# Kernel optimization log

Measured on AMD Instinct MI355X. Metric: run time of the kernel, lower is better.

## Reference

```python
import jax, jax.numpy as jnp
import numpy as np

SCALE = 2  # init_kwargs scale


def _splits(a, s):
    # (..., W, H) -> (..., W//s, H//s, s*s), matching torch view/permute order
    *lead, W, H = a.shape
    Ws, Hs = W // s, H // s
    n = len(lead)
    b = a.reshape(*lead, s, Ws, s, Hs)
    b = jnp.transpose(b, tuple(range(n)) + (n + 1, n + 3, n, n + 2))
    return b.reshape(*lead, Ws, Hs, s * s)


def _p2o(psf, shape):
    # point-spread-function -> optical transfer function (zero-pad, center-roll, fft2)
    k1, k2 = psf.shape[-2], psf.shape[-1]
    otf = jnp.zeros(psf.shape[:-2] + shape, psf.dtype).at[..., :k1, :k2].set(psf)
    otf = jnp.roll(otf, (-(k1 // 2), -(k2 // 2)), axis=(-2, -1))
    return jnp.fft.fft2(otf, axes=(-2, -1))


def _upsample_zeros(x, s):
    if s == 1:
        return x
    B, C, H, W = x.shape
    return jnp.zeros((B, C, H * s, W * s), x.dtype).at[..., ::s, ::s].set(x)


def setup_inputs() -> dict:
    key = jax.random.key(0)
    k1, k2 = jax.random.split(key)
    B, C, H, W, K = 4, 64, 128, 128, 5
    x = jax.random.normal(k1, (B, C, H, W), jnp.float32)
    w = jax.random.normal(k2, (1, C, K, K), jnp.float32)
    # module init applies softmax over flattened kernel
    weight = jax.nn.softmax(w.reshape(1, C, -1), axis=-1).reshape(1, C, K, K)
    bias = jnp.zeros((1, C, 1, 1), jnp.float32)
    lambda_reg = jnp.full((1, 1, 1, 1), 0.1, jnp.float32)
    return {"x": x, "weight": weight, "bias": bias, "lambda_reg": lambda_reg}


def reference(x, weight, bias, lambda_reg):
    s = SCALE
    _, _, h, w = x.shape
    STy = _upsample_zeros(x, s)                      # [B,C,h*s,w*s] zero-interleaved
    if s != 1:
        x0 = jnp.repeat(jnp.repeat(x, s, axis=-2), s, axis=-1)  # nearest interp
    else:
        x0 = x
    FB = _p2o(weight, (h * s, w * s))                # [1,C,hs,ws] complex
    FBC = jnp.conj(FB)
    F2B = jnp.abs(FB) ** 2
    FBFy = FBC * jnp.fft.fft2(STy, axes=(-2, -1))
    FR = FBFy + jnp.fft.fft2(lambda_reg * x0, axes=(-2, -1))
    FBR = jnp.mean(_splits(FB * FR, s), axis=-1)     # [B,C,h,w] complex
    invW = jnp.mean(_splits(F2B, s), axis=-1)        # [1,C,h,w] real
    lambda_small = lambda_reg                        # scalar lambda: no split needed
    invWBR = FBR / (invW + lambda_small)
    FCBinvWBR = FBC * jnp.tile(invWBR, (1, 1, s, s))
    FX = (FR - FCBinvWBR) / lambda_reg
    out = jnp.real(jnp.fft.ifft2(FX, axes=(-2, -1)))
    return out + bias
```

## Files before the change

kernel.cpp:

```cpp
#include <hip/hip_runtime.h>
#include <math.h>


struct cx { float x, y; };
__device__ __forceinline__ cx cmul(cx a, cx b){ return cx{a.x*b.x - a.y*b.y, a.x*b.y + a.y*b.x}; }
__device__ __forceinline__ cx cadd(cx a, cx b){ return cx{a.x+b.x, a.y+b.y}; }
__device__ __forceinline__ cx csub(cx a, cx b){ return cx{a.x-b.x, a.y-b.y}; }
__device__ __forceinline__ cx cconj(cx a){ return cx{a.x, -a.y}; }
__device__ __forceinline__ cx cscale(cx a, float s){ return cx{a.x*s, a.y*s}; }

__device__ __forceinline__ float2 cmulf(float2 a, float2 b){
    return make_float2(a.x*b.x - a.y*b.y, a.x*b.y + a.y*b.x);
}
__device__ __forceinline__ float2 cmulcf(float2 a, float2 b){
    return make_float2(a.x*b.x + a.y*b.y, a.y*b.x - a.x*b.y);
}
__device__ __forceinline__ float2 caddf(float2 a, float2 b){ return make_float2(a.x+b.x, a.y+b.y); }
__device__ __forceinline__ float2 csubf(float2 a, float2 b){ return make_float2(a.x-b.x, a.y-b.y); }

__device__ __forceinline__ void barrier_lds(){
    __builtin_amdgcn_sched_barrier(0);
    asm volatile("s_waitcnt lgkmcnt(0)" ::: "memory");
    __builtin_amdgcn_s_barrier();
    __builtin_amdgcn_sched_barrier(0);
}

__global__ __launch_bounds__(256)
void precompute_K(const float* __restrict__ weight, const float* __restrict__ lam_ptr,
                  float2* __restrict__ KA, float2* __restrict__ KB)
{
    __shared__ float2 P[5 * 256];

    const int tid  = threadIdx.x;
    const int c    = blockIdx.x >> 5;
    const int slab = blockIdx.x & 31;

    const float* wc = weight + c*25;
    const float lam = lam_ptr[0];
    const float th  = -6.28318530717958647692f * (1.0f/256.0f);

    {
        float s1,c1, s2,c2;
        __sincosf(th * (float)tid,     &s1, &c1);
        __sincosf(th * (float)(2*tid), &s2, &c2);
        cx er[5] = { cx{c2,-s2}, cx{c1,-s1}, cx{1.f,0.f}, cx{c1,s1}, cx{c2,s2} };
        const int rs = (tid >> 1) | ((tid & 1) << 7);
        #pragma unroll
        for (int a = 0; a < 5; ++a) {
            float px = 0.f, py = 0.f;
            #pragma unroll
            for (int b = 0; b < 5; ++b) {
                float w = wc[a*5 + b];
                px += w * er[b].x;
                py += w * er[b].y;
            }
            P[a*256 + rs] = make_float2(px, py);
        }
    }
    __syncthreads();

    const float scale = 1.0f / 65536.0f;

    #pragma unroll 1
    for (int it = 0; it < 2; ++it) {
        const int p  = slab*512 + it*256 + tid;
        const int qb = p >> 7, rb = p & 127;
        const int q = (int)(__brev((unsigned)qb) >> 25);
        const int r = (int)(__brev((unsigned)rb) >> 25);
        const int rr = (r >> 1) | ((r & 1) << 7);

        float sq1,cq1, sq2,cq2;
        __sincosf(th * (float)q,     &sq1, &cq1);
        __sincosf(th * (float)(2*q), &sq2, &cq2);
        cx eq[5] = { cx{cq2,-sq2}, cx{cq1,-sq1}, cx{1.f,0.f}, cx{cq1,sq1}, cx{cq2,sq2} };

        cx F00{0.f,0.f}, F01{0.f,0.f}, F10{0.f,0.f}, F11{0.f,0.f};
        #pragma unroll
        for (int a = 0; a < 5; ++a) {
            float2 p0 = P[a*256 + rr];
            float2 p1 = P[a*256 + rr + 64];
            cx t0 = cmul(eq[a], cx{p0.x, p0.y});
            cx t1 = cmul(eq[a], cx{p1.x, p1.y});
            F00 = cadd(F00, t0); F01 = cadd(F01, t1);
            if (a & 1) { F10 = csub(F10, t0); F11 = csub(F11, t1); }
            else       { F10 = cadd(F10, t0); F11 = cadd(F11, t1); }
        }

        const float cq = cq1, sq = sq1, cr = 0.f, sr = 0.f;
        (void)cr; (void)sr;
        float sr1, cr1;
        __sincosf(th * (float)r, &sr1, &cr1);

        cx Du[2] = { cx{1.f+cq,  sq}, cx{1.f-cq, -sq} };
        cx Dv[2] = { cx{1.f+cr1,  sr1}, cx{1.f-cr1, -sr1} };
        cx Fm[2][2] = { {F00, F01}, {F10, F11} };
        cx R[2][2];
        float invW = 0.f;
        cx M{0.f,0.f};
        #pragma unroll
        for (int i = 0; i < 2; ++i)
          #pragma unroll
          for (int k = 0; k < 2; ++k) {
            cx fb = Fm[i][k];
            cx Rik = cadd(cconj(fb), cscale(cmul(Du[i], Dv[k]), lam));
            R[i][k] = Rik;
            invW += 0.25f * (fb.x*fb.x + fb.y*fb.y);
            M = cadd(M, cscale(cmul(fb, Rik), 0.25f));
          }
        cx V = cscale(M, 1.0f / (invW + lam));
        float inv_lam = 1.0f / lam;
        cx G[2][2];
        #pragma unroll
        for (int i = 0; i < 2; ++i)
          #pragma unroll
          for (int k = 0; k < 2; ++k)
            G[i][k] = cscale(csub(R[i][k], cmul(cconj(Fm[i][k]), V)), inv_lam);

        cx G00 = G[0][0], G01 = G[0][1], G10 = G[1][0], G11 = G[1][1];
        cx Gh00 = cadd(cadd(G00,G01), cadd(G10,G11));
        cx Gh01 = cadd(csub(G00,G01), csub(G10,G11));
        cx Gh10 = csub(cadd(G00,G01), cadd(G10,G11));
        cx Gh11 = csub(csub(G00,G01), csub(G10,G11));
        cx phq = cx{cq, -sq};
        cx phr = cx{cr1, -sr1};
        cx H0 = Gh00;
        cx H1 = cmul(Gh01, phr);
        cx H2 = cmul(Gh10, phq);
        cx H3 = cmul(Gh11, cmul(phq, phr));

        float2 kAv = make_float2((H0.x - H1.y)*scale, (H0.y + H1.x)*scale);
        float2 kBv = make_float2((H2.x - H3.y)*scale, (H2.y + H3.x)*scale);
        const int o = (c << 14) + p;
        KA[o] = kAv;
        KB[o] = kBv;
    }
}

#define ST2 129

template<int AXIS> __device__ __forceinline__ int laddr(int line, int i){
    return AXIS ? (i*ST2 + line) : (line*ST2 + i);
}

template<int AXIS, int S>
__device__ __forceinline__ void fwd_pair(float2* Sm, const float2* TW, int tid)
{
    const int h  = 64 >> S;
    const int hh = 32 >> S;
    #pragma unroll
    for (int it = 0; it < 4; ++it) {
        int qid  = it*1024 + tid;
        int line = qid & 127;
        int t    = qid >> 7;
        int blk  = t >> (5 - S);
        int j    = t & (hh - 1);
        int i0   = (blk << (7 - S)) + j;
        int a0 = laddr<AXIS>(line, i0);
        int a1 = laddr<AXIS>(line, i0 + hh);
        int a2 = laddr<AXIS>(line, i0 + h);
        int a3 = laddr<AXIS>(line, i0 + h + hh);
        float2 e0 = Sm[a0], e1 = Sm[a1], e2 = Sm[a2], e3 = Sm[a3];
        float2 w0 = TW[j << S], w1 = TW[(j << S) + 32], w2 = TW[j << (S + 1)];
        float2 u0 = caddf(e0, e2), d0 = cmulf(csubf(e0, e2), w0);
        float2 u1 = caddf(e1, e3), d1 = cmulf(csubf(e1, e3), w1);
        Sm[a0] = caddf(u0, u1);
        Sm[a1] = cmulf(csubf(u0, u1), w2);
        Sm[a2] = caddf(d0, d1);
        Sm[a3] = cmulf(csubf(d0, d1), w2);
    }
}

template<int AXIS, int S>
__device__ __forceinline__ void inv_pair(float2* Sm, const float2* TW, int tid)
{
    const int h = 1 << S;
    #pragma unroll
    for (int it = 0; it < 4; ++it) {
        int qid  = it*1024 + tid;
        int line = qid & 127;
        int t    = qid >> 7;
        int blk  = t >> S;
        int j    = t & (h - 1);
        int base = (blk << (S + 2)) + j;
        int a0 = laddr<AXIS>(line, base);
        int a1 = laddr<AXIS>(line, base + h);
        int a2 = laddr<AXIS>(line, base + 2*h);
        int a3 = laddr<AXIS>(line, base + 3*h);
        float2 e0 = Sm[a0], e1 = Sm[a1], e2 = Sm[a2], e3 = Sm[a3];
        float2 cw0 = TW[j << (6 - S)];
        float2 cw1 = TW[j << (5 - S)];
        float2 cw2 = TW[(j << (5 - S)) + 32];
        float2 t1 = cmulcf(e1, cw0);
        float2 A0 = caddf(e0, t1), A1 = csubf(e0, t1);
        float2 t2 = cmulcf(e3, cw0);
        float2 A2 = caddf(e2, t2), A3 = csubf(e2, t2);
        float2 u = cmulcf(A2, cw1);
        Sm[a0] = caddf(A0, u);
        Sm[a2] = csubf(A0, u);
        float2 v = cmulcf(A3, cw2);
        Sm[a1] = caddf(A1, v);
        Sm[a3] = csubf(A1, v);
    }
}

__global__ __launch_bounds__(1024)
void converse_main(const float* __restrict__ x, const float* __restrict__ bias,
                   const float2* __restrict__ KA, const float2* __restrict__ KB,
                   float* __restrict__ out)
{
    __shared__ float2 S[128 * ST2];
    __shared__ float2 TW[64];

    const int tid = threadIdx.x;
    const int bc  = blockIdx.x;
    const int c   = bc & 63;

    if (tid < 64) {
        float s_, c_;
        __sincosf(-6.28318530717958647692f * (float)tid * (1.0f/128.0f), &s_, &c_);
        TW[tid] = make_float2(c_, s_);
    }

    const float* xp = x + (size_t)bc * 16384;
    #pragma unroll
    for (int it = 0; it < 16; ++it) {
        int n = it * 1024 + tid;
        S[(n >> 7) * ST2 + (n & 127)] = make_float2(xp[n], 0.0f);
    }

    const float2* KpA = KA + (size_t)c * 16384;
    const float2* KpB = KB + (size_t)c * 16384;
    const int nn = tid & 127;
    const int t7 = tid >> 7;
    const int kbase = t7*256 + nn;
    float2 kr[16];
    #pragma unroll
    for (int it = 0; it < 8; ++it) {
        kr[2*it]   = KpA[it*2048 + kbase];
        kr[2*it+1] = KpA[it*2048 + kbase + 128];
    }
    barrier_lds();

    fwd_pair<0,0>(S, TW, tid); barrier_lds();
    fwd_pair<0,2>(S, TW, tid); barrier_lds();
    fwd_pair<0,4>(S, TW, tid); barrier_lds();
    #pragma unroll
    for (int it = 0; it < 8; ++it) {
        int g = it*1024 + tid;
        int line = g & 127, k = g >> 7;
        int a = line*ST2 + 2*k;
        float2 u = S[a], v = S[a+1];
        S[a]   = caddf(u, v);
        S[a+1] = csubf(u, v);
    }
    barrier_lds();

    fwd_pair<1,0>(S, TW, tid); barrier_lds();
    fwd_pair<1,2>(S, TW, tid); barrier_lds();
    fwd_pair<1,4>(S, TW, tid); barrier_lds();

    const float bv = bias[c];
    float* op = out + (size_t)bc * 65536;

    float2 sA[8], sB[8];
    #pragma unroll
    for (int it = 0; it < 8; ++it) {
        int j = it*8 + t7;
        int a = (2*j)*ST2 + nn;
        float2 u = S[a], v = S[a + ST2];
        float2 vA = caddf(u, v);
        float2 vB = csubf(u, v);
        sA[it] = vA;
        sB[it] = vB;
        float2 w0 = cmulf(vA, kr[2*it]);
        float2 w1 = cmulf(vB, kr[2*it+1]);
        S[a]       = caddf(w0, w1);
        S[a + ST2] = csubf(w0, w1);
    }
    barrier_lds();

    inv_pair<1,1>(S, TW, tid); barrier_lds();
    inv_pair<1,3>(S, TW, tid); barrier_lds();
    inv_pair<1,5>(S, TW, tid); barrier_lds();
    inv_pair<0,0>(S, TW, tid); barrier_lds();
    inv_pair<0,2>(S, TW, tid); barrier_lds();
    inv_pair<0,4>(S, TW, tid); barrier_lds();

    #pragma unroll
    for (int it = 0; it < 8; ++it) {
        int g = it*1024 + tid;
        int j = g & 63, m = g >> 6;
        int a = m*ST2 + j;
        float2 u = S[a], v = S[a + 64];
        float2 t = cmulcf(v, TW[j]);
        float2 o0 = caddf(u, t);
        float2 o1 = csubf(u, t);
        size_t ro = (size_t)(2*m) * 256;
        *(float2*)(op + ro + 2*j)       = make_float2(o0.x + bv, o0.y + bv);
        *(float2*)(op + ro + 2*j + 128) = make_float2(o1.x + bv, o1.y + bv);
    }
    barrier_lds();

    #pragma unroll
    for (int it = 0; it < 8; ++it) {
        int j = it*8 + t7;
        float2 kb0 = KpB[it*2048 + kbase];
        float2 kb1 = KpB[it*2048 + kbase + 128];
        float2 w0 = cmulf(sA[it], kb0);
        float2 w1 = cmulf(sB[it], kb1);
        int a = (2*j)*ST2 + nn;
        S[a]       = caddf(w0, w1);
        S[a + ST2] = csubf(w0, w1);
    }
    barrier_lds();

    inv_pair<1,1>(S, TW, tid); barrier_lds();
    inv_pair<1,3>(S, TW, tid); barrier_lds();
    inv_pair<1,5>(S, TW, tid); barrier_lds();
    inv_pair<0,0>(S, TW, tid); barrier_lds();
    inv_pair<0,2>(S, TW, tid); barrier_lds();
    inv_pair<0,4>(S, TW, tid); barrier_lds();

    #pragma unroll
    for (int it = 0; it < 8; ++it) {
        int g = it*1024 + tid;
        int j = g & 63, m = g >> 6;
        int a = m*ST2 + j;
        float2 u = S[a], v = S[a + 64];
        float2 t = cmulcf(v, TW[j]);
        float2 o0 = caddf(u, t);
        float2 o1 = csubf(u, t);
        size_t ro = (size_t)(2*m + 1) * 256;
        *(float2*)(op + ro + 2*j)       = make_float2(o0.x + bv, o0.y + bv);
        *(float2*)(op + ro + 2*j + 128) = make_float2(o1.x + bv, o1.y + bv);
    }
}

extern "C" void kernel_launch(void* const* d_in, const int* in_sizes, int n_in,
                              void* d_out, int out_size, void* d_ws, size_t ws_size,
                              hipStream_t stream)
{
    const float* x      = (const float*)d_in[0];
    const float* weight = (const float*)d_in[1];
    const float* bias   = (const float*)d_in[2];
    const float* lam    = (const float*)d_in[3];
    float* out = (float*)d_out;

    float2* KA = (float2*)d_ws;
    float2* KB = KA + (size_t)64 * 16384;

    hipLaunchKernelGGL(precompute_K, dim3(2048), dim3(256), 0, stream,
                       weight, lam, KA, KB);
    hipLaunchKernelGGL(converse_main, dim3(256), dim3(1024), 0, stream,
                       x, bias, KA, KB, out);
}
```

Baseline: 131.8 us.

## Simplify OTF filter algebra and spill part of saved spectra to LDS

The precompute kernel's per-frequency filter is rederived algebraically. Conjugate-symmetric tap pairs are combined, and the 2x2 aliasing solve is collapsed into a single scalar W applied to the conjugated Hadamard terms, which cuts complex multiplies. In the main kernel, three of the eight saved vB spectra per thread move from registers to a new 24KB shared buffer. This lowers register pressure in the 1024-thread block at the cost of extra LDS traffic and footprint. The algebra rewrite risks numerical differences if the identity is not exact.

```diff
diff --git a/kernel.cpp b/kernel.cpp
--- a/kernel.cpp
+++ b/kernel.cpp
@@ -18,6 +18,11 @@
 __device__ __forceinline__ float2 caddf(float2 a, float2 b){ return make_float2(a.x+b.x, a.y+b.y); }
 __device__ __forceinline__ float2 csubf(float2 a, float2 b){ return make_float2(a.x-b.x, a.y-b.y); }
 
+__device__ __forceinline__ cx conjpair(cx w, float2 A, float2 B){
+    return cx{ w.x*(A.x+B.x) + w.y*(A.y-B.y),
+               w.x*(A.y+B.y) - w.y*(A.x-B.x) };
+}
+
 __device__ __forceinline__ void barrier_lds(){
     __builtin_amdgcn_sched_barrier(0);
     asm volatile("s_waitcnt lgkmcnt(0)" ::: "memory");
@@ -37,6 +42,7 @@
 
     const float* wc = weight + c*25;
     const float lam = lam_ptr[0];
+    const float inv_lam = 1.0f / lam;
     const float th  = -6.28318530717958647692f * (1.0f/256.0f);
 
     {
@@ -69,64 +75,54 @@
         const int r = (int)(__brev((unsigned)rb) >> 25);
         const int rr = (r >> 1) | ((r & 1) << 7);
 
-        float sq1,cq1, sq2,cq2;
+        float sq1,cq1, sq2,cq2, sr1,cr1;
         __sincosf(th * (float)q,     &sq1, &cq1);
         __sincosf(th * (float)(2*q), &sq2, &cq2);
-        cx eq[5] = { cx{cq2,-sq2}, cx{cq1,-sq1}, cx{1.f,0.f}, cx{cq1,sq1}, cx{cq2,sq2} };
-
-        cx F00{0.f,0.f}, F01{0.f,0.f}, F10{0.f,0.f}, F11{0.f,0.f};
-        #pragma unroll
-        for (int a = 0; a < 5; ++a) {
-            float2 p0 = P[a*256 + rr];
-            float2 p1 = P[a*256 + rr + 64];
-            cx t0 = cmul(eq[a], cx{p0.x, p0.y});
-            cx t1 = cmul(eq[a], cx{p1.x, p1.y});
-            F00 = cadd(F00, t0); F01 = cadd(F01, t1);
-            if (a & 1) { F10 = csub(F10, t0); F11 = csub(F11, t1); }
-            else       { F10 = cadd(F10, t0); F11 = cadd(F11, t1); }
-        }
-
-        const float cq = cq1, sq = sq1, cr = 0.f, sr = 0.f;
-        (void)cr; (void)sr;
-        float sr1, cr1;
-        __sincosf(th * (float)r, &sr1, &cr1);
-
-        cx Du[2] = { cx{1.f+cq,  sq}, cx{1.f-cq, -sq} };
-        cx Dv[2] = { cx{1.f+cr1,  sr1}, cx{1.f-cr1, -sr1} };
-        cx Fm[2][2] = { {F00, F01}, {F10, F11} };
-        cx R[2][2];
-        float invW = 0.f;
-        cx M{0.f,0.f};
-        #pragma unroll
-        for (int i = 0; i < 2; ++i)
-          #pragma unroll
-          for (int k = 0; k < 2; ++k) {
-            cx fb = Fm[i][k];
-            cx Rik = cadd(cconj(fb), cscale(cmul(Du[i], Dv[k]), lam));
-            R[i][k] = Rik;
-            invW += 0.25f * (fb.x*fb.x + fb.y*fb.y);
-            M = cadd(M, cscale(cmul(fb, Rik), 0.25f));
-          }
-        cx V = cscale(M, 1.0f / (invW + lam));
-        float inv_lam = 1.0f / lam;
-        cx G[2][2];
-        #pragma unroll
-        for (int i = 0; i < 2; ++i)
-          #pragma unroll
-          for (int k = 0; k < 2; ++k)
-            G[i][k] = cscale(csub(R[i][k], cmul(cconj(Fm[i][k]), V)), inv_lam);
-
-        cx G00 = G[0][0], G01 = G[0][1], G10 = G[1][0], G11 = G[1][1];
-        cx Gh00 = cadd(cadd(G00,G01), cadd(G10,G11));
-        cx Gh01 = cadd(csub(G00,G01), csub(G10,G11));
-        cx Gh10 = csub(cadd(G00,G01), cadd(G10,G11));
-        cx Gh11 = csub(csub(G00,G01), csub(G10,G11));
-        cx phq = cx{cq, -sq};
-        cx phr = cx{cr1, -sr1};
-        cx H0 = Gh00;
-        cx H1 = cmul(Gh01, phr);
-        cx H2 = cmul(Gh10, phq);
-        cx H3 = cmul(Gh11, cmul(phq, phr));
+        __sincosf(th * (float)r,     &sr1, &cr1);
+        const cx w1{cq1, sq1};
+        const cx w2{cq2, sq2};
+        const cx wr{cr1, sr1};
+
+        float2 p0_0 = P[0*256+rr], p1_0 = P[0*256+rr+64];
+        float2 p0_1 = P[1*256+rr], p1_1 = P[1*256+rr+64];
+        float2 p0_2 = P[2*256+rr], p1_2 = P[2*256+rr+64];
+        float2 p0_3 = P[3*256+rr], p1_3 = P[3*256+rr+64];
+        float2 p0_4 = P[4*256+rr], p1_4 = P[4*256+rr+64];
+        cx B1 = conjpair(w1, p0_1, p0_3);
+        cx B2 = conjpair(w2, p0_0, p0_4);
+        cx m0 = cx{p0_2.x, p0_2.y};
+        cx F00 = cadd(cadd(m0, B1), B2);
+        cx F10 = cadd(csub(m0, B1), B2);
+        cx D1 = conjpair(w1, p1_1, p1_3);
+        cx D2 = conjpair(w2, p1_0, p1_4);
+        cx m1 = cx{p1_2.x, p1_2.y};
+        cx F01 = cadd(cadd(m1, D1), D2);
+        cx F11 = cadd(csub(m1, D1), D2);
+
+        float SF2 = F00.x*F00.x + F00.y*F00.y + F01.x*F01.x + F01.y*F01.y
+                  + F10.x*F10.x + F10.y*F10.y + F11.x*F11.x + F11.y*F11.y;
+        cx Du0{1.f+cq1,  sq1}, Du1{1.f-cq1, -sq1};
+        cx Dv0{1.f+cr1,  sr1}, Dv1{1.f-cr1, -sr1};
+        cx T = cadd(cmul(Du0, cadd(cmul(F00,Dv0), cmul(F01,Dv1))),
+                    cmul(Du1, cadd(cmul(F10,Dv0), cmul(F11,Dv1))));
+        float invW = 0.25f * SF2;
+        cx M{invW + 0.25f*lam*T.x, 0.25f*lam*T.y};
+        float idn = 1.0f / (invW + lam);
+        cx V{M.x*idn, M.y*idn};
+        cx W{(1.f - V.x)*inv_lam, -V.y*inv_lam};
+
+        cx Sa = cadd(F00,F01), Sb = cadd(F10,F11);
+        cx Da = csub(F00,F01), Db = csub(F10,F11);
+        cx C00 = cadd(Sa,Sb), C10 = csub(Sa,Sb);
+        cx C01 = cadd(Da,Db), C11 = csub(Da,Db);
+
+        cx WR  = cmul(W,  cconj(wr));
+        cx WQ  = cmul(W,  cconj(w1));
+        cx WQR = cmul(WQ, cconj(wr));
+        cx H0 = cadd(cmul(cconj(C00), W  ), cx{4.f,0.f});
+        cx H1 = cadd(cmul(cconj(C01), WR ), cx{4.f,0.f});
+        cx H2 = cadd(cmul(cconj(C10), WQ ), cx{4.f,0.f});
+        cx H3 = cadd(cmul(cconj(C11), WQR), cx{4.f,0.f});
 
         float2 kAv = make_float2((H0.x - H1.y)*scale, (H0.y + H1.x)*scale);
         float2 kBv = make_float2((H2.x - H3.y)*scale, (H2.y + H3.x)*scale);
@@ -210,6 +206,7 @@
 {
     __shared__ float2 S[128 * ST2];
     __shared__ float2 TW[64];
+    __shared__ float2 SB[3 * 1024];
 
     const int tid = threadIdx.x;
     const int bc  = blockIdx.x;
@@ -262,7 +259,7 @@
     const float bv = bias[c];
     float* op = out + (size_t)bc * 65536;
 
-    float2 sA[8], sB[8];
+    float2 sA[8], sB[5];
     #pragma unroll
     for (int it = 0; it < 8; ++it) {
         int j = it*8 + t7;
@@ -271,7 +268,8 @@
         float2 vA = caddf(u, v);
         float2 vB = csubf(u, v);
         sA[it] = vA;
-        sB[it] = vB;
+        if (it < 5) sB[it] = vB;
+        else        SB[(it-5)*1024 + tid] = vB;
         float2 w0 = cmulf(vA, kr[2*it]);
         float2 w1 = cmulf(vB, kr[2*it+1]);
         S[a]       = caddf(w0, w1);
@@ -306,8 +304,9 @@
         int j = it*8 + t7;
         float2 kb0 = KpB[it*2048 + kbase];
         float2 kb1 = KpB[it*2048 + kbase + 128];
+        float2 vB = (it < 5) ? sB[it] : SB[(it-5)*1024 + tid];
         float2 w0 = cmulf(sA[it], kb0);
-        float2 w1 = cmulf(sB[it], kb1);
+        float2 w1 = cmulf(vB, kb1);
         int a = (2*j)*ST2 + nn;
         S[a]       = caddf(w0, w1);
         S[a + ST2] = csubf(w0, w1);
```

Measured after the change: 131.3 us. Within noise of the previous version (-0.4%).
